# Optimization experiments

Measured on AMD Instinct MI355X. Metric: run time of the kernel, lower is better.

The kernel has to match this reference:

```python
import jax, jax.numpy as jnp
import numpy as np

HUGE_FLOAT = 1000.0
B, LATENT, N, EMB, NBOND = 256, 256, 64, 64, 5


def setup_inputs() -> dict:
    key = jax.random.key(0)
    ks = jax.random.split(key, 8)
    s1 = 1.0 / np.sqrt(LATENT)
    s2 = 1.0 / np.sqrt(2 * EMB)
    s3 = 1.0 / np.sqrt(EMB)
    return {
        "z": jax.random.normal(ks[0], (B, LATENT), dtype=jnp.float32),
        "num_real_atoms": jax.random.randint(ks[1], (B,), 1, N + 1, dtype=jnp.int32),
        "W_nodes": jax.random.uniform(ks[2], (LATENT, N * EMB), jnp.float32, -s1, s1),
        "b_nodes": jax.random.uniform(ks[3], (N * EMB,), jnp.float32, -s1, s1),
        "W1": jax.random.uniform(ks[4], (2 * EMB, EMB), jnp.float32, -s2, s2),
        "b1": jax.random.uniform(ks[5], (EMB,), jnp.float32, -s2, s2),
        "W2": jax.random.uniform(ks[6], (EMB, NBOND), jnp.float32, -s3, s3),
        "b2": jax.random.uniform(ks[7], (NBOND,), jnp.float32, -s3, s3),
    }


def reference(z, num_real_atoms, W_nodes, b_nodes, W1, b1, W2, b2):
    # z: (B, latent) -> node embeddings h: (B, N, emb)
    h = (z @ W_nodes + b_nodes).reshape(B, N, EMB)
    # edge MLP first layer on concat([h_i, h_j]) == h_i @ W1a + h_j @ W1b
    W1a, W1b = W1[:EMB], W1[EMB:]
    a = jnp.einsum("bne,ef->bnf", h, W1a)  # (B, N, emb)
    c = jnp.einsum("bne,ef->bnf", h, W1b)  # (B, N, emb)
    hidden = jax.nn.relu(a[:, :, None, :] + c[:, None, :, :] + b1)  # (B,N,N,emb)
    logits = jnp.einsum("bijf,fk->bijk", hidden, W2) + b2  # (B,N,N,5)
    # diagonal mask + padding mask (symmetric), constant fill per bond channel
    diag = jnp.eye(N, dtype=bool)  # (N,N)
    real = jnp.arange(N)[None, :] < num_real_atoms[:, None]  # (B,N)
    pad = ~real
    padding = pad[:, :, None] | pad[:, None, :]  # (B,N,N)
    mask = diag[None] | padding  # (B,N,N)
    fill = jnp.where(jnp.arange(NBOND) == NBOND - 1, HUGE_FLOAT, -HUGE_FLOAT).astype(logits.dtype)
    logits = jnp.where(mask[..., None], fill, logits)
    # symmetrize over node pair dims
    return 0.5 * (logits + jnp.swapaxes(logits, 1, 2))
```

## Files before the change

### kernel.cpp

```cpp
#include <hip/hip_runtime.h>
#include <hip/hip_bf16.h>

#define HUGEF 1000.0f

typedef __hip_bfloat16 bf16;
typedef __attribute__((ext_vector_type(8))) short short8;
typedef __attribute__((ext_vector_type(4))) float floatx4;
typedef __attribute__((ext_vector_type(2))) float float2v;

__device__ __forceinline__ ushort f2bf(float x) {
    return __bfloat16_as_ushort(__float2bfloat16(x));
}
__device__ __forceinline__ float b2f(bf16 x) { return __bfloat162float(x); }
__device__ __forceinline__ float2v relu2(float2v x) {
    float2v r; r.x = fmaxf(x.x, 0.f); r.y = fmaxf(x.y, 0.f); return r;
}
__device__ __forceinline__ float2v mk2(float x, float y) {
    float2v r; r.x = x; r.y = y; return r;
}

__global__ __launch_bounds__(256) void k_hac(
    const float* __restrict__ z, const float* __restrict__ Wn,
    const float* __restrict__ bn, const float* __restrict__ W1,
    const float* __restrict__ b1, bf16* __restrict__ a_ws,
    bf16* __restrict__ c_ws)
{
    __shared__ ushort zt[64][136];
    __shared__ ushort wnt[64][136];
    __shared__ ushort ht[64][72];
    __shared__ ushort w1at[64][72];
    __shared__ ushort w1bt[64][72];

    const int t = threadIdx.x;
    const int lane = t & 63;
    const int wv = t >> 6;
    const int l15 = lane & 15;
    const int quad = lane >> 4;
    const int atom = blockIdx.x;
    const int m0 = blockIdx.y * 64;
    const int n0 = atom * 64;

    {
        const int f = t & 63;
        const int g = t >> 6;
        #pragma unroll
        for (int qq = 0; qq < 4; ++qq) {
            int e = g * 16 + qq * 4;
            ushort4 va, vb;
            va.x = f2bf(W1[(e + 0) * 64 + f]);
            va.y = f2bf(W1[(e + 1) * 64 + f]);
            va.z = f2bf(W1[(e + 2) * 64 + f]);
            va.w = f2bf(W1[(e + 3) * 64 + f]);
            vb.x = f2bf(W1[(64 + e + 0) * 64 + f]);
            vb.y = f2bf(W1[(64 + e + 1) * 64 + f]);
            vb.z = f2bf(W1[(64 + e + 2) * 64 + f]);
            vb.w = f2bf(W1[(64 + e + 3) * 64 + f]);
            *(ushort4*)&w1at[f][e] = va;
            *(ushort4*)&w1bt[f][e] = vb;
        }
    }

    floatx4 acc1[4] = {};
    for (int kt = 0; kt < 256; kt += 128) {
        __syncthreads();
        #pragma unroll
        for (int r = 0; r < 8; ++r) {
            int q = t + 256 * r;
            int m = q >> 5, kk = (q & 31) * 4;
            float4 v = *(const float4*)&z[(m0 + m) * 256 + kt + kk];
            ushort4 u = {f2bf(v.x), f2bf(v.y), f2bf(v.z), f2bf(v.w)};
            *(ushort4*)&zt[m][kk] = u;
        }
        {
            int n = t & 63, g = t >> 6;
            #pragma unroll
            for (int qq = 0; qq < 8; ++qq) {
                int k = g * 32 + qq * 4;
                const float* p = &Wn[(size_t)(kt + k) * 4096 + n0 + n];
                ushort4 u = {f2bf(p[0]), f2bf(p[4096]),
                             f2bf(p[2 * 4096]), f2bf(p[3 * 4096])};
                *(ushort4*)&wnt[n][k] = u;
            }
        }
        __syncthreads();
        #pragma unroll
        for (int ks = 0; ks < 4; ++ks) {
            short8 a = *(const short8*)&zt[wv * 16 + l15][ks * 32 + quad * 8];
            #pragma unroll
            for (int nt = 0; nt < 4; ++nt) {
                short8 bf = *(const short8*)&wnt[nt * 16 + l15][ks * 32 + quad * 8];
                acc1[nt] = __builtin_amdgcn_mfma_f32_16x16x32_bf16(a, bf, acc1[nt], 0, 0, 0);
            }
        }
    }

    #pragma unroll
    for (int nt = 0; nt < 4; ++nt) {
        float bnv = bn[n0 + nt * 16 + l15];
        #pragma unroll
        for (int r = 0; r < 4; ++r)
            ht[wv * 16 + quad * 4 + r][nt * 16 + l15] = f2bf(acc1[nt][r] + bnv);
    }
    __syncthreads();

    floatx4 acc2a[4] = {}, acc2c[4] = {};
    #pragma unroll
    for (int ks = 0; ks < 2; ++ks) {
        short8 a = *(const short8*)&ht[wv * 16 + l15][ks * 32 + quad * 8];
        #pragma unroll
        for (int ft = 0; ft < 4; ++ft) {
            short8 ba = *(const short8*)&w1at[ft * 16 + l15][ks * 32 + quad * 8];
            short8 bb = *(const short8*)&w1bt[ft * 16 + l15][ks * 32 + quad * 8];
            acc2a[ft] = __builtin_amdgcn_mfma_f32_16x16x32_bf16(a, ba, acc2a[ft], 0, 0, 0);
            acc2c[ft] = __builtin_amdgcn_mfma_f32_16x16x32_bf16(a, bb, acc2c[ft], 0, 0, 0);
        }
    }

    #pragma unroll
    for (int ft = 0; ft < 4; ++ft) {
        float b1v = b1[ft * 16 + l15];
        #pragma unroll
        for (int r = 0; r < 4; ++r) {
            int m = wv * 16 + quad * 4 + r;
            size_t idx = (size_t)(m0 + m) * 4096 + n0 + ft * 16 + l15;
            a_ws[idx] = __float2bfloat16(acc2a[ft][r] + b1v);
            c_ws[idx] = __float2bfloat16(acc2c[ft][r]);
        }
    }
}

__global__ __launch_bounds__(256) void k_pairs(
    const bf16* __restrict__ a_ws, const bf16* __restrict__ c_ws,
    const int* __restrict__ nra, const float* __restrict__ W2,
    const float* __restrict__ b2, float* __restrict__ out)
{
    __shared__ __align__(16) float as[64][68];
    __shared__ __align__(16) float cs[64][68];
    __shared__ __align__(16) float w2t[5][68];

    const int t = threadIdx.x;
    const int b = blockIdx.x >> 1;
    const int ic = blockIdx.x & 1;
    const int n = nra[b];

    #pragma unroll
    for (int r = 0; r < 4; ++r) {
        int q = t + 256 * r;
        int atom = q >> 4, ff = (q & 15) * 4;
        ushort4 av = *(const ushort4*)((const ushort*)a_ws + (size_t)b * 4096 + 4 * q);
        ushort4 cv = *(const ushort4*)((const ushort*)c_ws + (size_t)b * 4096 + 4 * q);
        as[atom][ff + 0] = b2f(__ushort_as_bfloat16(av.x));
        as[atom][ff + 1] = b2f(__ushort_as_bfloat16(av.y));
        as[atom][ff + 2] = b2f(__ushort_as_bfloat16(av.z));
        as[atom][ff + 3] = b2f(__ushort_as_bfloat16(av.w));
        cs[atom][ff + 0] = b2f(__ushort_as_bfloat16(cv.x));
        cs[atom][ff + 1] = b2f(__ushort_as_bfloat16(cv.y));
        cs[atom][ff + 2] = b2f(__ushort_as_bfloat16(cv.z));
        cs[atom][ff + 3] = b2f(__ushort_as_bfloat16(cv.w));
    }
    if (t < 64) {
        #pragma unroll
        for (int k = 0; k < 5; ++k) w2t[k][t] = W2[t * 5 + k];
    }
    float b2v[5];
    #pragma unroll
    for (int k = 0; k < 5; ++k) b2v[k] = b2[k];
    __syncthreads();

    const int j = t & 63;
    const int wv = t >> 6;
    const int i0 = ic * 32 + wv * 8;
    const float fillv[5] = {-HUGEF, -HUGEF, -HUGEF, -HUGEF, HUGEF};

    if (i0 >= n) {
        #pragma unroll
        for (int r = 0; r < 8; ++r) {
            float* op = out + ((size_t)(b * 64 + i0 + r) * 64 + j) * 5;
            #pragma unroll
            for (int k = 0; k < 5; ++k) op[k] = fillv[k];
        }
        return;
    }

    float2v acc2[8][5] = {};
    for (int w8 = 0; w8 < 8; ++w8) {
        const int f0 = w8 * 8;
        float4 ajA = *(const float4*)&as[j][f0];
        float4 ajB = *(const float4*)&as[j][f0 + 4];
        float4 cjA = *(const float4*)&cs[j][f0];
        float4 cjB = *(const float4*)&cs[j][f0 + 4];
        float2v aj0 = mk2(ajA.x, ajA.y), aj1 = mk2(ajA.z, ajA.w);
        float2v aj2 = mk2(ajB.x, ajB.y), aj3 = mk2(ajB.z, ajB.w);
        float2v cj0 = mk2(cjA.x, cjA.y), cj1 = mk2(cjA.z, cjA.w);
        float2v cj2 = mk2(cjB.x, cjB.y), cj3 = mk2(cjB.z, cjB.w);
        float2v w[5][4];
        #pragma unroll
        for (int k = 0; k < 5; ++k) {
            float4 wA = *(const float4*)&w2t[k][f0];
            float4 wB = *(const float4*)&w2t[k][f0 + 4];
            w[k][0] = mk2(wA.x, wA.y); w[k][1] = mk2(wA.z, wA.w);
            w[k][2] = mk2(wB.x, wB.y); w[k][3] = mk2(wB.z, wB.w);
        }
        #pragma unroll
        for (int r = 0; r < 8; ++r) {
            float4 aiA = *(const float4*)&as[i0 + r][f0];
            float4 aiB = *(const float4*)&as[i0 + r][f0 + 4];
            float4 ciA = *(const float4*)&cs[i0 + r][f0];
            float4 ciB = *(const float4*)&cs[i0 + r][f0 + 4];
            float2v s0 = relu2(mk2(aiA.x, aiA.y) + cj0) + relu2(aj0 + mk2(ciA.x, ciA.y));
            float2v s1 = relu2(mk2(aiA.z, aiA.w) + cj1) + relu2(aj1 + mk2(ciA.z, ciA.w));
            float2v s2 = relu2(mk2(aiB.x, aiB.y) + cj2) + relu2(aj2 + mk2(ciB.x, ciB.y));
            float2v s3 = relu2(mk2(aiB.z, aiB.w) + cj3) + relu2(aj3 + mk2(ciB.z, ciB.w));
            #pragma unroll
            for (int k = 0; k < 5; ++k)
                acc2[r][k] += s0 * w[k][0] + s1 * w[k][1] +
                              s2 * w[k][2] + s3 * w[k][3];
        }
    }

    #pragma unroll
    for (int r = 0; r < 8; ++r) {
        const int i = i0 + r;
        float* op = out + ((size_t)(b * 64 + i) * 64 + j) * 5;
        if (i >= n) {
            #pragma unroll
            for (int k = 0; k < 5; ++k) op[k] = fillv[k];
        } else {
            const bool masked = (j == i) || (j >= n);
            #pragma unroll
            for (int k = 0; k < 5; ++k) {
                float v = masked ? fillv[k]
                                 : (0.5f * (acc2[r][k].x + acc2[r][k].y) + b2v[k]);
                op[k] = v;
            }
        }
    }
}

extern "C" void kernel_launch(void* const* d_in, const int* in_sizes, int n_in,
                              void* d_out, int out_size, void* d_ws, size_t ws_size,
                              hipStream_t stream)
{
    const float* z  = (const float*)d_in[0];
    const int*   nra = (const int*)d_in[1];
    const float* Wn = (const float*)d_in[2];
    const float* bn = (const float*)d_in[3];
    const float* W1 = (const float*)d_in[4];
    const float* b1 = (const float*)d_in[5];
    const float* W2 = (const float*)d_in[6];
    const float* b2 = (const float*)d_in[7];
    float* out = (float*)d_out;

    bf16* a_ws = (bf16*)d_ws;
    bf16* c_ws = a_ws + 256 * 4096;

    hipLaunchKernelGGL(k_hac, dim3(64, 4), dim3(256), 0, stream,
                       z, Wn, bn, W1, b1, a_ws, c_ws);
    hipLaunchKernelGGL(k_pairs, dim3(512), dim3(256), 0, stream,
                       a_ws, c_ws, nra, W2, b2, out);
}
```

Baseline: 100.9 us.

## Halve k_hac M-tile to 32 rows and process a whole batch per k_pairs block

k_hac now tiles 32 batch rows per block instead of 64, doubling the grid to 512 blocks. Its four waves split into a 2x2 arrangement over rows and output column tiles, and a min-blocks-per-CU hint of 2 is added. k_pairs now uses one block per batch element, with each wave looping over two 8-row i groups, so the a/c tiles are loaded once per batch rather than twice. This trades fewer k_pairs blocks, and so less parallelism and coarser padding-based load balance, for less redundant staging, while k_hac gains more blocks to fill the GPU at the cost of re-staging the Wn tile more often.

```diff
diff --git a/kernel.cpp b/kernel.cpp
--- a/kernel.cpp
+++ b/kernel.cpp
@@ -19,15 +19,15 @@
     float2v r; r.x = x; r.y = y; return r;
 }
 
-__global__ __launch_bounds__(256) void k_hac(
+__global__ __launch_bounds__(256, 2) void k_hac(
     const float* __restrict__ z, const float* __restrict__ Wn,
     const float* __restrict__ bn, const float* __restrict__ W1,
     const float* __restrict__ b1, bf16* __restrict__ a_ws,
     bf16* __restrict__ c_ws)
 {
-    __shared__ ushort zt[64][136];
+    __shared__ ushort zt[32][136];
     __shared__ ushort wnt[64][136];
-    __shared__ ushort ht[64][72];
+    __shared__ ushort ht[32][72];
     __shared__ ushort w1at[64][72];
     __shared__ ushort w1bt[64][72];
 
@@ -37,8 +37,10 @@
     const int l15 = lane & 15;
     const int quad = lane >> 4;
     const int atom = blockIdx.x;
-    const int m0 = blockIdx.y * 64;
+    const int m0 = blockIdx.y * 32;
     const int n0 = atom * 64;
+    const int mrow = (wv >> 1) * 16;
+    const int ntb = (wv & 1) * 2;
 
     {
         const int f = t & 63;
@@ -60,11 +62,11 @@
         }
     }
 
-    floatx4 acc1[4] = {};
+    floatx4 acc1[2] = {};
     for (int kt = 0; kt < 256; kt += 128) {
         __syncthreads();
         #pragma unroll
-        for (int r = 0; r < 8; ++r) {
+        for (int r = 0; r < 4; ++r) {
             int q = t + 256 * r;
             int m = q >> 5, kk = (q & 31) * 4;
             float4 v = *(const float4*)&z[(m0 + m) * 256 + kt + kk];
@@ -85,46 +87,46 @@
         __syncthreads();
         #pragma unroll
         for (int ks = 0; ks < 4; ++ks) {
-            short8 a = *(const short8*)&zt[wv * 16 + l15][ks * 32 + quad * 8];
-            #pragma unroll
-            for (int nt = 0; nt < 4; ++nt) {
-                short8 bf = *(const short8*)&wnt[nt * 16 + l15][ks * 32 + quad * 8];
-                acc1[nt] = __builtin_amdgcn_mfma_f32_16x16x32_bf16(a, bf, acc1[nt], 0, 0, 0);
-            }
-        }
-    }
-
-    #pragma unroll
-    for (int nt = 0; nt < 4; ++nt) {
-        float bnv = bn[n0 + nt * 16 + l15];
+            short8 a = *(const short8*)&zt[mrow + l15][ks * 32 + quad * 8];
+            #pragma unroll
+            for (int p = 0; p < 2; ++p) {
+                short8 bf = *(const short8*)&wnt[(ntb + p) * 16 + l15][ks * 32 + quad * 8];
+                acc1[p] = __builtin_amdgcn_mfma_f32_16x16x32_bf16(a, bf, acc1[p], 0, 0, 0);
+            }
+        }
+    }
+
+    #pragma unroll
+    for (int p = 0; p < 2; ++p) {
+        float bnv = bn[n0 + (ntb + p) * 16 + l15];
         #pragma unroll
         for (int r = 0; r < 4; ++r)
-            ht[wv * 16 + quad * 4 + r][nt * 16 + l15] = f2bf(acc1[nt][r] + bnv);
+            ht[mrow + quad * 4 + r][(ntb + p) * 16 + l15] = f2bf(acc1[p][r] + bnv);
     }
     __syncthreads();
 
-    floatx4 acc2a[4] = {}, acc2c[4] = {};
+    floatx4 acc2a[2] = {}, acc2c[2] = {};
     #pragma unroll
     for (int ks = 0; ks < 2; ++ks) {
-        short8 a = *(const short8*)&ht[wv * 16 + l15][ks * 32 + quad * 8];
-        #pragma unroll
-        for (int ft = 0; ft < 4; ++ft) {
-            short8 ba = *(const short8*)&w1at[ft * 16 + l15][ks * 32 + quad * 8];
-            short8 bb = *(const short8*)&w1bt[ft * 16 + l15][ks * 32 + quad * 8];
-            acc2a[ft] = __builtin_amdgcn_mfma_f32_16x16x32_bf16(a, ba, acc2a[ft], 0, 0, 0);
-            acc2c[ft] = __builtin_amdgcn_mfma_f32_16x16x32_bf16(a, bb, acc2c[ft], 0, 0, 0);
-        }
-    }
-
-    #pragma unroll
-    for (int ft = 0; ft < 4; ++ft) {
-        float b1v = b1[ft * 16 + l15];
+        short8 a = *(const short8*)&ht[mrow + l15][ks * 32 + quad * 8];
+        #pragma unroll
+        for (int p = 0; p < 2; ++p) {
+            short8 ba = *(const short8*)&w1at[(ntb + p) * 16 + l15][ks * 32 + quad * 8];
+            short8 bb = *(const short8*)&w1bt[(ntb + p) * 16 + l15][ks * 32 + quad * 8];
+            acc2a[p] = __builtin_amdgcn_mfma_f32_16x16x32_bf16(a, ba, acc2a[p], 0, 0, 0);
+            acc2c[p] = __builtin_amdgcn_mfma_f32_16x16x32_bf16(a, bb, acc2c[p], 0, 0, 0);
+        }
+    }
+
+    #pragma unroll
+    for (int p = 0; p < 2; ++p) {
+        float b1v = b1[(ntb + p) * 16 + l15];
         #pragma unroll
         for (int r = 0; r < 4; ++r) {
-            int m = wv * 16 + quad * 4 + r;
-            size_t idx = (size_t)(m0 + m) * 4096 + n0 + ft * 16 + l15;
-            a_ws[idx] = __float2bfloat16(acc2a[ft][r] + b1v);
-            c_ws[idx] = __float2bfloat16(acc2c[ft][r]);
+            int m = mrow + quad * 4 + r;
+            size_t idx = (size_t)(m0 + m) * 4096 + n0 + (ntb + p) * 16 + l15;
+            a_ws[idx] = __float2bfloat16(acc2a[p][r] + b1v);
+            c_ws[idx] = __float2bfloat16(acc2c[p][r]);
         }
     }
 }
@@ -139,8 +141,7 @@
     __shared__ __align__(16) float w2t[5][68];
 
     const int t = threadIdx.x;
-    const int b = blockIdx.x >> 1;
-    const int ic = blockIdx.x & 1;
+    const int b = blockIdx.x;
     const int n = nra[b];
 
     #pragma unroll
@@ -169,69 +170,72 @@
 
     const int j = t & 63;
     const int wv = t >> 6;
-    const int i0 = ic * 32 + wv * 8;
     const float fillv[5] = {-HUGEF, -HUGEF, -HUGEF, -HUGEF, HUGEF};
 
-    if (i0 >= n) {
+    #pragma unroll 1
+    for (int oo = 0; oo < 2; ++oo) {
+        const int i0 = (wv + 4 * oo) * 8;
+        if (i0 >= n) {
+            #pragma unroll
+            for (int r = 0; r < 8; ++r) {
+                float* op = out + ((size_t)(b * 64 + i0 + r) * 64 + j) * 5;
+                #pragma unroll
+                for (int k = 0; k < 5; ++k) op[k] = fillv[k];
+            }
+            continue;
+        }
+
+        float2v acc2[8][5] = {};
+        for (int w8 = 0; w8 < 8; ++w8) {
+            const int f0 = w8 * 8;
+            float4 ajA = *(const float4*)&as[j][f0];
+            float4 ajB = *(const float4*)&as[j][f0 + 4];
+            float4 cjA = *(const float4*)&cs[j][f0];
+            float4 cjB = *(const float4*)&cs[j][f0 + 4];
+            float2v aj0 = mk2(ajA.x, ajA.y), aj1 = mk2(ajA.z, ajA.w);
+            float2v aj2 = mk2(ajB.x, ajB.y), aj3 = mk2(ajB.z, ajB.w);
+            float2v cj0 = mk2(cjA.x, cjA.y), cj1 = mk2(cjA.z, cjA.w);
+            float2v cj2 = mk2(cjB.x, cjB.y), cj3 = mk2(cjB.z, cjB.w);
+            float2v w[5][4];
+            #pragma unroll
+            for (int k = 0; k < 5; ++k) {
+                float4 wA = *(const float4*)&w2t[k][f0];
+                float4 wB = *(const float4*)&w2t[k][f0 + 4];
+                w[k][0] = mk2(wA.x, wA.y); w[k][1] = mk2(wA.z, wA.w);
+                w[k][2] = mk2(wB.x, wB.y); w[k][3] = mk2(wB.z, wB.w);
+            }
+            #pragma unroll
+            for (int r = 0; r < 8; ++r) {
+                float4 aiA = *(const float4*)&as[i0 + r][f0];
+                float4 aiB = *(const float4*)&as[i0 + r][f0 + 4];
+                float4 ciA = *(const float4*)&cs[i0 + r][f0];
+                float4 ciB = *(const float4*)&cs[i0 + r][f0 + 4];
+                float2v s0 = relu2(mk2(aiA.x, aiA.y) + cj0) + relu2(aj0 + mk2(ciA.x, ciA.y));
+                float2v s1 = relu2(mk2(aiA.z, aiA.w) + cj1) + relu2(aj1 + mk2(ciA.z, ciA.w));
+                float2v s2 = relu2(mk2(aiB.x, aiB.y) + cj2) + relu2(aj2 + mk2(ciB.x, ciB.y));
+                float2v s3 = relu2(mk2(aiB.z, aiB.w) + cj3) + relu2(aj3 + mk2(ciB.z, ciB.w));
+                #pragma unroll
+                for (int k = 0; k < 5; ++k)
+                    acc2[r][k] += s0 * w[k][0] + s1 * w[k][1] +
+                                  s2 * w[k][2] + s3 * w[k][3];
+            }
+        }
+
         #pragma unroll
         for (int r = 0; r < 8; ++r) {
-            float* op = out + ((size_t)(b * 64 + i0 + r) * 64 + j) * 5;
-            #pragma unroll
-            for (int k = 0; k < 5; ++k) op[k] = fillv[k];
-        }
-        return;
-    }
-
-    float2v acc2[8][5] = {};
-    for (int w8 = 0; w8 < 8; ++w8) {
-        const int f0 = w8 * 8;
-        float4 ajA = *(const float4*)&as[j][f0];
-        float4 ajB = *(const float4*)&as[j][f0 + 4];
-        float4 cjA = *(const float4*)&cs[j][f0];
-        float4 cjB = *(const float4*)&cs[j][f0 + 4];
-        float2v aj0 = mk2(ajA.x, ajA.y), aj1 = mk2(ajA.z, ajA.w);
-        float2v aj2 = mk2(ajB.x, ajB.y), aj3 = mk2(ajB.z, ajB.w);
-        float2v cj0 = mk2(cjA.x, cjA.y), cj1 = mk2(cjA.z, cjA.w);
-        float2v cj2 = mk2(cjB.x, cjB.y), cj3 = mk2(cjB.z, cjB.w);
-        float2v w[5][4];
-        #pragma unroll
-        for (int k = 0; k < 5; ++k) {
-            float4 wA = *(const float4*)&w2t[k][f0];
-            float4 wB = *(const float4*)&w2t[k][f0 + 4];
-            w[k][0] = mk2(wA.x, wA.y); w[k][1] = mk2(wA.z, wA.w);
-            w[k][2] = mk2(wB.x, wB.y); w[k][3] = mk2(wB.z, wB.w);
-        }
-        #pragma unroll
-        for (int r = 0; r < 8; ++r) {
-            float4 aiA = *(const float4*)&as[i0 + r][f0];
-            float4 aiB = *(const float4*)&as[i0 + r][f0 + 4];
-            float4 ciA = *(const float4*)&cs[i0 + r][f0];
-            float4 ciB = *(const float4*)&cs[i0 + r][f0 + 4];
-            float2v s0 = relu2(mk2(aiA.x, aiA.y) + cj0) + relu2(aj0 + mk2(ciA.x, ciA.y));
-            float2v s1 = relu2(mk2(aiA.z, aiA.w) + cj1) + relu2(aj1 + mk2(ciA.z, ciA.w));
-            float2v s2 = relu2(mk2(aiB.x, aiB.y) + cj2) + relu2(aj2 + mk2(ciB.x, ciB.y));
-            float2v s3 = relu2(mk2(aiB.z, aiB.w) + cj3) + relu2(aj3 + mk2(ciB.z, ciB.w));
-            #pragma unroll
-            for (int k = 0; k < 5; ++k)
-                acc2[r][k] += s0 * w[k][0] + s1 * w[k][1] +
-                              s2 * w[k][2] + s3 * w[k][3];
-        }
-    }
-
-    #pragma unroll
-    for (int r = 0; r < 8; ++r) {
-        const int i = i0 + r;
-        float* op = out + ((size_t)(b * 64 + i) * 64 + j) * 5;
-        if (i >= n) {
-            #pragma unroll
-            for (int k = 0; k < 5; ++k) op[k] = fillv[k];
-        } else {
-            const bool masked = (j == i) || (j >= n);
-            #pragma unroll
-            for (int k = 0; k < 5; ++k) {
-                float v = masked ? fillv[k]
-                                 : (0.5f * (acc2[r][k].x + acc2[r][k].y) + b2v[k]);
-                op[k] = v;
+            const int i = i0 + r;
+            float* op = out + ((size_t)(b * 64 + i) * 64 + j) * 5;
+            if (i >= n) {
+                #pragma unroll
+                for (int k = 0; k < 5; ++k) op[k] = fillv[k];
+            } else {
+                const bool masked = (j == i) || (j >= n);
+                #pragma unroll
+                for (int k = 0; k < 5; ++k) {
+                    float v = masked ? fillv[k]
+                                     : (0.5f * (acc2[r][k].x + acc2[r][k].y) + b2v[k]);
+                    op[k] = v;
+                }
             }
         }
     }
@@ -254,8 +258,8 @@
     bf16* a_ws = (bf16*)d_ws;
     bf16* c_ws = a_ws + 256 * 4096;
 
-    hipLaunchKernelGGL(k_hac, dim3(64, 4), dim3(256), 0, stream,
+    hipLaunchKernelGGL(k_hac, dim3(64, 8), dim3(256), 0, stream,
                        z, Wn, bn, W1, b1, a_ws, c_ws);
-    hipLaunchKernelGGL(k_pairs, dim3(512), dim3(256), 0, stream,
+    hipLaunchKernelGGL(k_pairs, dim3(256), dim3(256), 0, stream,
                        a_ws, c_ws, nra, W2, b2, out);
 }
```

Result: slower. 105.1 us (+4.2%).
